# Optimization experiments

Measured on AMD Instinct MI355X. Metric: run time of the kernel, lower is better.

The kernel has to match this reference:

```python
import jax, jax.numpy as jnp
import numpy as np

K, D, N = 32, 64, 65536
LOG_2PI = float(np.log(2.0 * np.pi))


def setup_inputs() -> dict:
    key = jax.random.key(0)
    k1, k2, k3, k4 = jax.random.split(key, 4)
    X = jax.random.normal(k1, (N, D), dtype=jnp.float32)
    loc = jax.random.normal(k2, (K, D), dtype=jnp.float32)
    # SPD full covariances per component: A A^T + I
    A = 0.1 * jax.random.normal(k3, (K, D, D), dtype=jnp.float32)
    cov = jnp.einsum('kij,klj->kil', A, A) + jnp.eye(D, dtype=jnp.float32)
    pi = jax.random.normal(k4, (K,), dtype=jnp.float32)
    return {"X": X, "loc": loc, "cov": cov, "pi": pi}


def _gmm_log_prob(X, loc, cov, pi):
    d = X.shape[-1]
    L = jnp.linalg.cholesky(cov)                       # [K, d, d]
    diff = X[:, None, :] - loc[None, :, :]             # [N, K, d]
    # per-component triangular solve: z_k = L_k^{-1} (x - mu_k)
    solve = lambda Lk, dk: jax.scipy.linalg.solve_triangular(Lk, dk.T, lower=True)  # [d, N]
    z = jax.vmap(solve, in_axes=(0, 1))(L, diff)       # [K, d, N]
    maha = jnp.sum(z * z, axis=1).T                    # [N, K]
    half_logdet = jnp.sum(jnp.log(jnp.diagonal(L, axis1=-2, axis2=-1)), axis=-1)  # [K]
    comp_logp = -0.5 * (d * LOG_2PI + maha) - half_logdet[None, :]  # [N, K]
    # Categorical(softmax(pi)).logits followed by log_softmax == log_softmax(pi)
    weighted = comp_logp + jax.nn.log_softmax(pi)[None, :]
    return jax.scipy.special.logsumexp(weighted, axis=1, keepdims=True)  # [N, 1]


def reference(X, loc, cov, pi):
    return _gmm_log_prob(X, loc, cov, pi)
```

## Files before the change

### kernel.cpp

```cpp
#include <hip/hip_runtime.h>
#include <math.h>

#define KCOMP 32
#define DDIM 64
#define LOG_2PI 1.8378770664093453f

#define WFRAG_HALF8S 64
#define WCOMP_BYTES 10240

typedef _Float16 half8 __attribute__((ext_vector_type(8)));
typedef float floatx16 __attribute__((ext_vector_type(16)));
typedef float float2v __attribute__((ext_vector_type(2)));

__device__ inline float rdlane(float v, int l) {
    return __uint_as_float(__builtin_amdgcn_readlane(__float_as_uint(v), l));
}

template <int J>
__device__ __forceinline__ void fused_step(float (&Srow)[DDIM], float2v (&LM)[DDIM],
                                           float& mydiag, const int t) {
    constexpr int NB8  = J / 8;
    constexpr int REM  = J - NB8 * 8;
    constexpr int TAIL = (REM == 0) ? 0 : (REM <= 4 ? 4 : 8);
    float2v am[8];
    #pragma unroll
    for (int e = 0; e < 8; ++e) am[e] = (float2v){0.f, 0.f};
    #pragma unroll
    for (int p8 = 0; p8 < NB8 * 8; p8 += 8) {
        float b[8];
        #pragma unroll
        for (int e = 0; e < 8; ++e) b[e] = rdlane(LM[p8 + e].x, J);
        #pragma unroll
        for (int e = 0; e < 8; ++e) {
            float2v bb = {b[e], b[e]};
            am[e] += LM[p8 + e] * bb;
        }
    }
    if constexpr (TAIL > 0) {
        constexpr int base = NB8 * 8;
        float b[8];
        #pragma unroll
        for (int e = 0; e < TAIL; ++e) b[e] = rdlane(LM[base + e].x, J);
        #pragma unroll
        for (int e = 0; e < TAIL; ++e) {
            float2v bb = {b[e], b[e]};
            am[e] += LM[base + e] * bb;
        }
    }
    float2v red = ((am[0] + am[1]) + (am[2] + am[3]))
                + ((am[4] + am[5]) + (am[6] + am[7]));
    float dot = red.x;
    float ms  = red.y;
    float v  = Srow[J] - dot;
    float dj = rdlane(v, J);
    float r  = rsqrtf(dj);
    float lv = (t >= J) ? v * r : 0.f;
    float mv = (t < J) ? (-ms * r) : ((t == J) ? r : 0.f);
    LM[J] = (float2v){lv, mv};
    if (t == J) mydiag = dj;
}

template <int J>
__device__ __forceinline__ void fused_run(float (&Srow)[DDIM], float2v (&LM)[DDIM],
                                          float& mydiag, const int t) {
    fused_step<J>(Srow, LM, mydiag, t);
    if constexpr (J + 1 < DDIM) fused_run<J + 1>(Srow, LM, mydiag, t);
}

__global__ __launch_bounds__(64, 1) void gmm_prep(const float* __restrict__ loc,
                                                  const float* __restrict__ cov,
                                                  const float* __restrict__ pi,
                                                  _Float16* __restrict__ wt,
                                                  float* __restrict__ cstout)
{
    const int k = blockIdx.x;
    const int t = threadIdx.x;

    __shared__ float M[DDIM][DDIM + 1];
    __shared__ float mu_s[DDIM];

    float Srow[DDIM];
    float2v LM[DDIM];

    {
        const float4* Sg = (const float4*)(cov + (size_t)k * DDIM * DDIM + (size_t)t * DDIM);
        #pragma unroll
        for (int q = 0; q < DDIM / 4; ++q) {
            float4 v = Sg[q];
            Srow[q * 4 + 0] = v.x; Srow[q * 4 + 1] = v.y;
            Srow[q * 4 + 2] = v.z; Srow[q * 4 + 3] = v.w;
        }
    }
    #pragma unroll
    for (int i = 0; i < DDIM; ++i) LM[i] = (float2v){0.f, 0.f};
    mu_s[t] = loc[k * DDIM + t];

    float mydiag = 1.f;
    fused_run<0>(Srow, LM, mydiag, t);

    float hld;
    {
        float lg = 0.5f * logf(mydiag);
        #pragma unroll
        for (int w = 1; w < 64; w <<= 1) lg += __shfl_xor(lg, w);
        hld = lg;
    }

    #pragma unroll
    for (int i = 0; i < DDIM; ++i) M[i][t] = LM[i].y;
    __syncthreads();

    float bt = 0.f;
    #pragma unroll 4
    for (int j = 0; j < DDIM; ++j) bt += M[t][j] * mu_s[j];

    {
        const int r = t >> 5, lrow = t & 31;
        half8* wp = (half8*)wt;
        const size_t fbase = ((size_t)k * 2 + r) * 5;
        #pragma unroll
        for (int c = 0; c < 8; ++c) {
            half8 v;
            #pragma unroll
            for (int e = 0; e < 8; ++e) v[e] = (_Float16)M[t][c * 8 + e];
            int fl = lrow + 32 * (c & 1);
            wp[(fbase + (c >> 1)) * WFRAG_HALF8S + fl] = v;
        }
        {
            float nb = -bt;
            _Float16 h0 = (_Float16)nb;
            _Float16 h1 = (_Float16)(nb - (float)h0);
            half8 v;
            #pragma unroll
            for (int e = 0; e < 8; ++e) v[e] = (_Float16)0.f;
            v[0] = h0; v[1] = h1;
            wp[(fbase + 4) * WFRAG_HALF8S + lrow] = v;
        }
        {
            half8 v;
            #pragma unroll
            for (int e = 0; e < 8; ++e) v[e] = (_Float16)0.f;
            wp[(fbase + 4) * WFRAG_HALF8S + lrow + 32] = v;
        }
    }

    if (t == 0) {
        float mxp = pi[0];
        for (int i = 1; i < KCOMP; ++i) mxp = fmaxf(mxp, pi[i]);
        float s = 0.f;
        for (int i = 0; i < KCOMP; ++i) s += __expf(pi[i] - mxp);
        float lse = mxp + logf(s);
        cstout[k] = (pi[k] - lse) - hld - 0.5f * (float)DDIM * LOG_2PI;
    }
}

__global__ __launch_bounds__(256, 1) void gmm_main(const float* __restrict__ X,
                                                   const _Float16* __restrict__ wt,
                                                   const float* __restrict__ cst,
                                                   float* __restrict__ out)
{
    __shared__ float2 part[4][128];

    const int tid  = threadIdx.x;
    const int wave = tid >> 6;
    const int lane = tid & 63;
    const int col  = lane & 31;
    const int h    = lane >> 5;
    const int ptbase = blockIdx.x * 128;

    half8 bf[4][5];
    #pragma unroll
    for (int g = 0; g < 4; ++g) {
        const float* xr = X + (size_t)(ptbase + g * 32 + col) * DDIM;
        #pragma unroll
        for (int s = 0; s < 4; ++s) {
            int c = s * 2 + h;
            float4 lo = *(const float4*)(xr + c * 8);
            float4 hi = *(const float4*)(xr + c * 8 + 4);
            half8 v;
            v[0] = (_Float16)lo.x; v[1] = (_Float16)lo.y;
            v[2] = (_Float16)lo.z; v[3] = (_Float16)lo.w;
            v[4] = (_Float16)hi.x; v[5] = (_Float16)hi.y;
            v[6] = (_Float16)hi.z; v[7] = (_Float16)hi.w;
            bf[g][s] = v;
        }
        half8 v;
        #pragma unroll
        for (int e = 0; e < 8; ++e) v[e] = (_Float16)0.f;
        if (h == 0) { v[0] = (_Float16)1.f; v[1] = (_Float16)1.f; }
        bf[g][4] = v;
    }

    const half8* wp = (const half8*)wt;
    const int comp0 = wave * 8;

    float mx[4], sm[4];
    #pragma unroll
    for (int g = 0; g < 4; ++g) { mx[g] = -INFINITY; sm[g] = 0.f; }

    half8 wfA[5], wfB[5];
    #pragma unroll
    for (int s = 0; s < 5; ++s)
        wfA[s] = wp[((size_t)comp0 * 2 + 0) * 5 * WFRAG_HALF8S + s * WFRAG_HALF8S + lane];

    #pragma unroll 1
    for (int q = 0; q < 8; ++q) {
        const int c = comp0 + q;

        #pragma unroll
        for (int s = 0; s < 5; ++s)
            wfB[s] = wp[((size_t)c * 2 + 1) * 5 * WFRAG_HALF8S + s * WFRAG_HALF8S + lane];

        float sP[4];

        {
            floatx16 a0 = {0.f}, a1 = {0.f}, a2 = {0.f}, a3 = {0.f};
            #pragma unroll
            for (int s = 0; s < 5; ++s) {
                a0 = __builtin_amdgcn_mfma_f32_32x32x16_f16(wfA[s], bf[0][s], a0, 0, 0, 0);
                a1 = __builtin_amdgcn_mfma_f32_32x32x16_f16(wfA[s], bf[1][s], a1, 0, 0, 0);
                a2 = __builtin_amdgcn_mfma_f32_32x32x16_f16(wfA[s], bf[2][s], a2, 0, 0, 0);
                a3 = __builtin_amdgcn_mfma_f32_32x32x16_f16(wfA[s], bf[3][s], a3, 0, 0, 0);
            }
            float p0 = 0.f, p1 = 0.f, p2 = 0.f, p3 = 0.f;
            #pragma unroll
            for (int r = 0; r < 16; ++r) {
                p0 += a0[r] * a0[r]; p1 += a1[r] * a1[r];
                p2 += a2[r] * a2[r]; p3 += a3[r] * a3[r];
            }
            sP[0] = p0; sP[1] = p1; sP[2] = p2; sP[3] = p3;
        }

        if (q < 7) {
            #pragma unroll
            for (int s = 0; s < 5; ++s)
                wfA[s] = wp[((size_t)(c + 1) * 2 + 0) * 5 * WFRAG_HALF8S + s * WFRAG_HALF8S + lane];
        }

        {
            floatx16 a0 = {0.f}, a1 = {0.f}, a2 = {0.f}, a3 = {0.f};
            #pragma unroll
            for (int s = 0; s < 5; ++s) {
                a0 = __builtin_amdgcn_mfma_f32_32x32x16_f16(wfB[s], bf[0][s], a0, 0, 0, 0);
                a1 = __builtin_amdgcn_mfma_f32_32x32x16_f16(wfB[s], bf[1][s], a1, 0, 0, 0);
                a2 = __builtin_amdgcn_mfma_f32_32x32x16_f16(wfB[s], bf[2][s], a2, 0, 0, 0);
                a3 = __builtin_amdgcn_mfma_f32_32x32x16_f16(wfB[s], bf[3][s], a3, 0, 0, 0);
            }
            float p0 = 0.f, p1 = 0.f, p2 = 0.f, p3 = 0.f;
            #pragma unroll
            for (int r = 0; r < 16; ++r) {
                p0 += a0[r] * a0[r]; p1 += a1[r] * a1[r];
                p2 += a2[r] * a2[r]; p3 += a3[r] * a3[r];
            }
            sP[0] += p0; sP[1] += p1; sP[2] += p2; sP[3] += p3;
        }

        const float ck = cst[c];
        #pragma unroll
        for (int g = 0; g < 4; ++g) {
            float sfull = sP[g] + __shfl_xor(sP[g], 32);
            float lp = ck - 0.5f * sfull;
            float nm = fmaxf(mx[g], lp);
            sm[g] = sm[g] * __expf(mx[g] - nm) + __expf(lp - nm);
            mx[g] = nm;
        }
    }

    if (h == 0) {
        #pragma unroll
        for (int g = 0; g < 4; ++g)
            part[wave][g * 32 + col] = make_float2(mx[g], sm[g]);
    }
    __syncthreads();

    if (tid < 128) {
        float2 p0 = part[0][tid], p1 = part[1][tid];
        float2 p2 = part[2][tid], p3 = part[3][tid];
        float m = fmaxf(fmaxf(p0.x, p1.x), fmaxf(p2.x, p3.x));
        float s = p0.y * __expf(p0.x - m) + p1.y * __expf(p1.x - m)
                + p2.y * __expf(p2.x - m) + p3.y * __expf(p3.x - m);
        out[ptbase + tid] = m + logf(s);
    }
}

extern "C" void kernel_launch(void* const* d_in, const int* in_sizes, int n_in,
                              void* d_out, int out_size, void* d_ws, size_t ws_size,
                              hipStream_t stream) {
    const float* X   = (const float*)d_in[0];
    const float* loc = (const float*)d_in[1];
    const float* cov = (const float*)d_in[2];
    const float* pi  = (const float*)d_in[3];
    float* out = (float*)d_out;

    char* ws = (char*)d_ws;
    _Float16* wt = (_Float16*)ws;
    float* cstp  = (float*)(ws + (size_t)KCOMP * WCOMP_BYTES);

    const int n = in_sizes[0] / DDIM;

    gmm_prep<<<KCOMP, 64, 0, stream>>>(loc, cov, pi, wt, cstp);
    gmm_main<<<n / 128, 256, 0, stream>>>(X, wt, cstp, out);
}
```

Before: 46.03 us.

## Interleave two Cholesky factorizations per prep wave to hide latency

The prep kernel now handles two mixture components per 64-thread block, interleaving their sequential Cholesky/inverse recurrences so the two independent dependency chains can overlap readlane and FMA latency. Covariance row entries are streamed from global memory one step ahead instead of being held in a register array, which frees registers for the second component's state. The grid is halved, so fewer CUs are used for the latency-bound prep phase. Register pressure could cause spills.

```diff
diff --git a/kernel.cpp b/kernel.cpp
--- a/kernel.cpp
+++ b/kernel.cpp
@@ -17,97 +17,105 @@
 }
 
 template <int J>
-__device__ __forceinline__ void fused_step(float (&Srow)[DDIM], float2v (&LM)[DDIM],
-                                           float& mydiag, const int t) {
+__device__ __forceinline__ void fused_step2(const float* __restrict__ sgA,
+                                            const float* __restrict__ sgB,
+                                            float2v (&LA)[DDIM], float2v (&LB)[DDIM],
+                                            float& diagA, float& diagB,
+                                            float& sA, float& sB, const int t) {
+    float snA = 0.f, snB = 0.f;
+    if constexpr (J + 1 < DDIM) {
+        snA = sgA[J + 1];
+        snB = sgB[J + 1];
+    }
+
     constexpr int NB8  = J / 8;
     constexpr int REM  = J - NB8 * 8;
     constexpr int TAIL = (REM == 0) ? 0 : (REM <= 4 ? 4 : 8);
-    float2v am[8];
-    #pragma unroll
-    for (int e = 0; e < 8; ++e) am[e] = (float2v){0.f, 0.f};
+
+    float2v aA0 = {0.f,0.f}, aA1 = {0.f,0.f}, aA2 = {0.f,0.f}, aA3 = {0.f,0.f};
+    float2v aB0 = {0.f,0.f}, aB1 = {0.f,0.f}, aB2 = {0.f,0.f}, aB3 = {0.f,0.f};
+
     #pragma unroll
     for (int p8 = 0; p8 < NB8 * 8; p8 += 8) {
-        float b[8];
-        #pragma unroll
-        for (int e = 0; e < 8; ++e) b[e] = rdlane(LM[p8 + e].x, J);
+        float bA[8], bB[8];
+        #pragma unroll
+        for (int e = 0; e < 8; ++e) bA[e] = rdlane(LA[p8 + e].x, J);
+        #pragma unroll
+        for (int e = 0; e < 8; ++e) bB[e] = rdlane(LB[p8 + e].x, J);
         #pragma unroll
         for (int e = 0; e < 8; ++e) {
-            float2v bb = {b[e], b[e]};
-            am[e] += LM[p8 + e] * bb;
+            float2v bbA = {bA[e], bA[e]};
+            float2v bbB = {bB[e], bB[e]};
+            switch (e & 3) {
+                case 0: aA0 += LA[p8 + e] * bbA; aB0 += LB[p8 + e] * bbB; break;
+                case 1: aA1 += LA[p8 + e] * bbA; aB1 += LB[p8 + e] * bbB; break;
+                case 2: aA2 += LA[p8 + e] * bbA; aB2 += LB[p8 + e] * bbB; break;
+                default: aA3 += LA[p8 + e] * bbA; aB3 += LB[p8 + e] * bbB; break;
+            }
         }
     }
     if constexpr (TAIL > 0) {
         constexpr int base = NB8 * 8;
-        float b[8];
-        #pragma unroll
-        for (int e = 0; e < TAIL; ++e) b[e] = rdlane(LM[base + e].x, J);
+        float bA[8], bB[8];
+        #pragma unroll
+        for (int e = 0; e < TAIL; ++e) bA[e] = rdlane(LA[base + e].x, J);
+        #pragma unroll
+        for (int e = 0; e < TAIL; ++e) bB[e] = rdlane(LB[base + e].x, J);
         #pragma unroll
         for (int e = 0; e < TAIL; ++e) {
-            float2v bb = {b[e], b[e]};
-            am[e] += LM[base + e] * bb;
-        }
-    }
-    float2v red = ((am[0] + am[1]) + (am[2] + am[3]))
-                + ((am[4] + am[5]) + (am[6] + am[7]));
-    float dot = red.x;
-    float ms  = red.y;
-    float v  = Srow[J] - dot;
-    float dj = rdlane(v, J);
-    float r  = rsqrtf(dj);
-    float lv = (t >= J) ? v * r : 0.f;
-    float mv = (t < J) ? (-ms * r) : ((t == J) ? r : 0.f);
-    LM[J] = (float2v){lv, mv};
-    if (t == J) mydiag = dj;
+            float2v bbA = {bA[e], bA[e]};
+            float2v bbB = {bB[e], bB[e]};
+            switch (e & 3) {
+                case 0: aA0 += LA[base + e] * bbA; aB0 += LB[base + e] * bbB; break;
+                case 1: aA1 += LA[base + e] * bbA; aB1 += LB[base + e] * bbB; break;
+                case 2: aA2 += LA[base + e] * bbA; aB2 += LB[base + e] * bbB; break;
+                default: aA3 += LA[base + e] * bbA; aB3 += LB[base + e] * bbB; break;
+            }
+        }
+    }
+
+    float2v redA = (aA0 + aA1) + (aA2 + aA3);
+    float2v redB = (aB0 + aB1) + (aB2 + aB3);
+
+    float vA = sA - redA.x;
+    float vB = sB - redB.x;
+    float djA = rdlane(vA, J);
+    float djB = rdlane(vB, J);
+    float rA = rsqrtf(djA);
+    float rB = rsqrtf(djB);
+    float lvA = (t >= J) ? vA * rA : 0.f;
+    float lvB = (t >= J) ? vB * rB : 0.f;
+    float mvA = (t < J) ? (-redA.y * rA) : ((t == J) ? rA : 0.f);
+    float mvB = (t < J) ? (-redB.y * rB) : ((t == J) ? rB : 0.f);
+    LA[J] = (float2v){lvA, mvA};
+    LB[J] = (float2v){lvB, mvB};
+    if (t == J) { diagA = djA; diagB = djB; }
+    sA = snA;
+    sB = snB;
 }
 
 template <int J>
-__device__ __forceinline__ void fused_run(float (&Srow)[DDIM], float2v (&LM)[DDIM],
-                                          float& mydiag, const int t) {
-    fused_step<J>(Srow, LM, mydiag, t);
-    if constexpr (J + 1 < DDIM) fused_run<J + 1>(Srow, LM, mydiag, t);
-}
-
-__global__ __launch_bounds__(64, 1) void gmm_prep(const float* __restrict__ loc,
-                                                  const float* __restrict__ cov,
-                                                  const float* __restrict__ pi,
-                                                  _Float16* __restrict__ wt,
-                                                  float* __restrict__ cstout)
-{
-    const int k = blockIdx.x;
-    const int t = threadIdx.x;
-
-    __shared__ float M[DDIM][DDIM + 1];
-    __shared__ float mu_s[DDIM];
-
-    float Srow[DDIM];
-    float2v LM[DDIM];
-
-    {
-        const float4* Sg = (const float4*)(cov + (size_t)k * DDIM * DDIM + (size_t)t * DDIM);
-        #pragma unroll
-        for (int q = 0; q < DDIM / 4; ++q) {
-            float4 v = Sg[q];
-            Srow[q * 4 + 0] = v.x; Srow[q * 4 + 1] = v.y;
-            Srow[q * 4 + 2] = v.z; Srow[q * 4 + 3] = v.w;
-        }
-    }
-    #pragma unroll
-    for (int i = 0; i < DDIM; ++i) LM[i] = (float2v){0.f, 0.f};
+__device__ __forceinline__ void fused_run2(const float* __restrict__ sgA,
+                                           const float* __restrict__ sgB,
+                                           float2v (&LA)[DDIM], float2v (&LB)[DDIM],
+                                           float& diagA, float& diagB,
+                                           float& sA, float& sB, const int t) {
+    fused_step2<J>(sgA, sgB, LA, LB, diagA, diagB, sA, sB, t);
+    if constexpr (J + 1 < DDIM)
+        fused_run2<J + 1>(sgA, sgB, LA, LB, diagA, diagB, sA, sB, t);
+}
+
+__device__ __forceinline__ void emit_comp(const int k, const int t,
+                                          const float2v (&LM)[DDIM], float mydiag,
+                                          const float* __restrict__ loc,
+                                          const float* __restrict__ pi,
+                                          _Float16* __restrict__ wt,
+                                          float* __restrict__ cstout,
+                                          float (*M)[DDIM + 1],
+                                          float* __restrict__ mu_s) {
+    #pragma unroll
+    for (int i = 0; i < DDIM; ++i) M[i][t] = LM[i].y;
     mu_s[t] = loc[k * DDIM + t];
-
-    float mydiag = 1.f;
-    fused_run<0>(Srow, LM, mydiag, t);
-
-    float hld;
-    {
-        float lg = 0.5f * logf(mydiag);
-        #pragma unroll
-        for (int w = 1; w < 64; w <<= 1) lg += __shfl_xor(lg, w);
-        hld = lg;
-    }
-
-    #pragma unroll
-    for (int i = 0; i < DDIM; ++i) M[i][t] = LM[i].y;
     __syncthreads();
 
     float bt = 0.f;
@@ -144,6 +152,13 @@
         }
     }
 
+    float hld;
+    {
+        float lg = 0.5f * logf(mydiag);
+        #pragma unroll
+        for (int w = 1; w < 64; w <<= 1) lg += __shfl_xor(lg, w);
+        hld = lg;
+    }
     if (t == 0) {
         float mxp = pi[0];
         for (int i = 1; i < KCOMP; ++i) mxp = fmaxf(mxp, pi[i]);
@@ -152,6 +167,41 @@
         float lse = mxp + logf(s);
         cstout[k] = (pi[k] - lse) - hld - 0.5f * (float)DDIM * LOG_2PI;
     }
+    __syncthreads();
+}
+
+__global__ __launch_bounds__(64, 1) void gmm_prep(const float* __restrict__ loc,
+                                                  const float* __restrict__ cov,
+                                                  const float* __restrict__ pi,
+                                                  _Float16* __restrict__ wt,
+                                                  float* __restrict__ cstout)
+{
+    const int kA = blockIdx.x * 2;
+    const int kB = kA + 1;
+    const int t  = threadIdx.x;
+
+    __shared__ float M[DDIM][DDIM + 1];
+    __shared__ float mu_s[DDIM];
+
+    float2v LA[DDIM];
+    float2v LB[DDIM];
+
+    #pragma unroll
+    for (int i = 0; i < DDIM; ++i) {
+        LA[i] = (float2v){0.f, 0.f};
+        LB[i] = (float2v){0.f, 0.f};
+    }
+
+    const float* sgA = cov + (size_t)kA * DDIM * DDIM + (size_t)t * DDIM;
+    const float* sgB = cov + (size_t)kB * DDIM * DDIM + (size_t)t * DDIM;
+
+    float diagA = 1.f, diagB = 1.f;
+    float sA = sgA[0], sB = sgB[0];
+
+    fused_run2<0>(sgA, sgB, LA, LB, diagA, diagB, sA, sB, t);
+
+    emit_comp(kA, t, LA, diagA, loc, pi, wt, cstout, M, mu_s);
+    emit_comp(kB, t, LB, diagB, loc, pi, wt, cstout, M, mu_s);
 }
 
 __global__ __launch_bounds__(256, 1) void gmm_main(const float* __restrict__ X,
@@ -298,6 +348,6 @@
 
     const int n = in_sizes[0] / DDIM;
 
-    gmm_prep<<<KCOMP, 64, 0, stream>>>(loc, cov, pi, wt, cstp);
+    gmm_prep<<<KCOMP / 2, 64, 0, stream>>>(loc, cov, pi, wt, cstp);
     gmm_main<<<n / 128, 256, 0, stream>>>(X, wt, cstp, out);
 }
```

Result: slower. 72.46 us (+57.4%).
